# Optimization experiments

Measured on AMD Instinct MI355X. Metric: run time of the kernel, lower is better.

## Reference

```python
import jax, jax.numpy as jnp
import numpy as np

HEAD = 4
EPS = 1e-12


def _l2norm(x, axis):
    # torch F.normalize: x / max(||x||_2, eps)
    return x / jnp.maximum(jnp.linalg.norm(x, axis=axis, keepdims=True), EPS)


def setup_inputs() -> dict:
    key = jax.random.key(0)
    ks = jax.random.split(key, 12)
    n, t, c, h, w = 2, 7, 96, 96, 96
    inp = {
        "curr_feat": jax.random.normal(ks[0], (n, c, h, w), jnp.float32),
        "index_feat_set_s1": jax.random.normal(ks[1], (n, t, c, h, w), jnp.float32),
        "anchor_feat": jax.random.normal(ks[2], (n, c, h, w), jnp.float32),
        "sparse_feat_set_s1": jax.random.normal(ks[3], (n, t, c, h, w), jnp.float32),
        "sparse_feat_set_s2": jax.random.normal(ks[4], (n, t, c, h, w), jnp.float32),
        "sparse_feat_set_s3": jax.random.normal(ks[5], (n, t, c, h, w), jnp.float32),
        # absolute pixel coordinates (x,y interleaved per frame), mostly in-bounds
        # with a little overshoot to exercise zeros padding of grid_sample
        "location_feat": jax.random.uniform(ks[6], (n, t * 2, h, w), jnp.float32, minval=-2.0, maxval=float(w) + 1.0),
        "proj_w": 0.02 * jax.random.normal(ks[7], (c, c), jnp.float32),
        "proj_b": jnp.zeros((c,), jnp.float32),
        "fusion_w": 0.02 * jax.random.normal(ks[8], (c, 3 * c), jnp.float32),
        "fusion_b": jnp.zeros((c,), jnp.float32),
    }
    return inp


def reference(curr_feat, index_feat_set_s1, anchor_feat, sparse_feat_set_s1,
              sparse_feat_set_s2, sparse_feat_set_s3, location_feat,
              proj_w, proj_b, fusion_w, fusion_b):
    n, c, h, w = anchor_feat.shape
    t = sparse_feat_set_s1.shape[1]
    hd = c // HEAD
    hw = h * w

    # ---- flow-guided nearest grid_sample (align_corners=True, zeros pad) ----
    loc = location_feat.reshape(n, t, 2, h, w)  # (n,t,2,h,w): [x, y] pixel coords
    gx = 2.0 * loc[:, :, 0] / max(w - 1, 1) - 1.0
    gy = 2.0 * loc[:, :, 1] / max(h - 1, 1) - 1.0
    ix = jnp.round((gx + 1.0) * 0.5 * (w - 1))  # nearest (round-half-even, as torch)
    iy = jnp.round((gy + 1.0) * 0.5 * (h - 1))
    valid = (ix >= 0) & (ix <= w - 1) & (iy >= 0) & (iy <= h - 1)
    lin = (jnp.clip(iy, 0, h - 1).astype(jnp.int32) * w
           + jnp.clip(ix, 0, w - 1).astype(jnp.int32)).reshape(n, t, 1, hw)
    vmask = valid.reshape(n, t, 1, hw)

    def sample(f):  # f: (n,t,c,h,w) -> gathered (n,t,c,hw)
        g = jnp.take_along_axis(f.reshape(n, t, c, hw), lin, axis=3)
        return jnp.where(vmask, g, 0.0)

    samp1 = sample(sparse_feat_set_s1)
    samp2 = sample(sparse_feat_set_s2)
    samp3 = sample(sparse_feat_set_s3)
    sampi = sample(index_feat_set_s1)

    # ---- per-pixel multi-head max-correlation over t frames ----
    # queries: normalize over full channel dim c BEFORE splitting into heads
    q = _l2norm(curr_feat.reshape(n, c, hw).transpose(0, 2, 1), -1).reshape(n, hw, HEAD, hd)
    k = _l2norm(sampi.transpose(0, 3, 1, 2), -1).reshape(n, hw, t, HEAD, hd)
    scores = jnp.einsum('npthd,nphd->npht', k, q)  # scale == 1.0 in mode='max'
    corr_soft = jnp.max(scores, axis=3)     # (n,hw,head)
    corr_index = jnp.argmax(scores, axis=3)  # (n,hw,head), first-max like torch

    soft_img = jnp.broadcast_to(corr_soft[..., None], (n, hw, HEAD, hd)) \
                  .reshape(n, h, w, c).transpose(0, 3, 1, 2)  # (n,c,h,w)
    idx = jnp.broadcast_to(corr_index[..., None], (n, hw, HEAD, hd)) \
             .reshape(n, hw, c).transpose(0, 2, 1)[:, None]  # (n,1,c,hw)

    def pick(samp):  # select winning frame per (channel-group, pixel)
        return jnp.take_along_axis(samp, idx, axis=1)[:, 0].reshape(n, c, h, w)

    cat = jnp.concatenate([pick(samp1), pick(samp2), pick(samp3)], axis=1)  # (n,3c,h,w)
    out = jnp.einsum('ndhw,cd->nchw', cat, fusion_w) + fusion_b[None, :, None, None]
    out = out * soft_img
    out = jnp.einsum('nchw,dc->ndhw', out, proj_w) + proj_b[None, :, None, None]
    return out + anchor_feat
```

## Files before the change

### kernel.cpp

```cpp
#include <hip/hip_runtime.h>
#include <hip/hip_bf16.h>

#define N_    2
#define T_    7
#define C_    96
#define H_    96
#define W_    96
#define HW_   9216
#define HEAD_ 4
#define HD_   24
#define C3_   288
#define P_    16
#define QP_   100
#define CATP_ 292
#define NBLK_ (N_ * (HW_ / P_))
#define PLANES_ 14
#define CHUNK_  64
#define NCHUNK_ 144
#define TBLK_ (PLANES_ * NCHUNK_)

typedef unsigned int u32;

__device__ __forceinline__ float bits2f(u32 b) {
    union { u32 u; float f; } x; x.u = b; return x.f;
}

__device__ __forceinline__ unsigned short f2bf(float f) {
    union { __hip_bfloat16 h; unsigned short s; } u;
    u.h = __float2bfloat16(f);
    return u.s;
}

template<bool BF16>
__device__ __forceinline__ float ld1(const void* p, int i) {
    if constexpr (BF16) return bits2f(((u32)((const unsigned short*)p)[i]) << 16);
    else                return ((const float*)p)[i];
}

template<bool BF16>
__device__ __forceinline__ void ld4w(const void* p, int i, float w[4]) {
    if constexpr (BF16) {
        const uint2 u = ((const uint2*)p)[i >> 2];
        w[0] = bits2f(u.x << 16);
        w[1] = bits2f(u.x & 0xFFFF0000u);
        w[2] = bits2f(u.y << 16);
        w[3] = bits2f(u.y & 0xFFFF0000u);
    } else {
        const float4 v = *((const float4*)((const float*)p + i));
        w[0] = v.x; w[1] = v.y; w[2] = v.z; w[3] = v.w;
    }
}

template<bool BF16>
__device__ __forceinline__ void st1(void* p, int i, float v) {
    if constexpr (BF16) ((unsigned short*)p)[i] = f2bf(v);
    else                ((float*)p)[i] = v;
}

template<bool BF16>
__device__ __forceinline__ void st4w(void* p, int i, const float v[4]) {
    if constexpr (BF16) {
        uint2 w;
        w.x = (u32)f2bf(v[0]) | ((u32)f2bf(v[1]) << 16);
        w.y = (u32)f2bf(v[2]) | ((u32)f2bf(v[3]) << 16);
        ((uint2*)p)[i >> 2] = w;
    } else {
        *((float4*)((float*)p + i)) = make_float4(v[0], v[1], v[2], v[3]);
    }
}

__device__ __forceinline__ bool block_detect_bf16(const u32* __restrict__ w,
                                                  int tid, int* s_flag) {
    if (tid < 64) {
        u32 x = w[tid];
        u32 f = x & 0x7FFFu;
        int inwin = (f >= 0x3A00u) && (f <= 0x4200u);
        unsigned long long m = __ballot(inwin);
        if (tid == 0) *s_flag = (__popcll(m) >= 40) ? 1 : 0;
    }
    __syncthreads();
    return *s_flag != 0;
}

template<bool BF16>
__device__ __forceinline__ void transp_swz(const void* __restrict__ src,
                                           void* __restrict__ dst,
                                           int pl, int x0, int tid, char* raw) {
    if constexpr (BF16) {
        unsigned short* tile = (unsigned short*)raw;
        const unsigned short* s = (const unsigned short*)src;
        unsigned short* d = (unsigned short*)dst;
        for (int i = tid; i < C_ * (CHUNK_ / 4); i += 256) {
            int ch = i >> 4, xq = i & 15;
            const ushort4 v = *((const ushort4*)(s + (pl * C_ + ch) * HW_ + x0 + 4 * xq));
            int g = (ch >> 2) ^ (xq & 7);
            int chl = ch & 3;
            tile[(4 * xq + 0) * 96 + 4 * g + chl] = v.x;
            tile[(4 * xq + 1) * 96 + 4 * g + chl] = v.y;
            tile[(4 * xq + 2) * 96 + 4 * g + chl] = v.z;
            tile[(4 * xq + 3) * 96 + 4 * g + chl] = v.w;
        }
        __syncthreads();
        for (int i = tid; i < CHUNK_ * (C_ / 4); i += 256) {
            int p = i / 24, cq = i - p * 24;
            int g = cq ^ ((p >> 2) & 7);
            const ushort4 v = *((const ushort4*)&tile[p * 96 + 4 * g]);
            *((ushort4*)(d + (pl * HW_ + x0 + p) * C_ + 4 * cq)) = v;
        }
    } else {
        float* tile = (float*)raw;
        const float* s = (const float*)src;
        float* d = (float*)dst;
        for (int i = tid; i < C_ * (CHUNK_ / 4); i += 256) {
            int ch = i >> 4, xq = i & 15;
            const float4 v = *((const float4*)(s + (pl * C_ + ch) * HW_ + x0 + 4 * xq));
            int g = (ch >> 2) ^ (xq & 7);
            int chl = ch & 3;
            tile[(4 * xq + 0) * 96 + 4 * g + chl] = v.x;
            tile[(4 * xq + 1) * 96 + 4 * g + chl] = v.y;
            tile[(4 * xq + 2) * 96 + 4 * g + chl] = v.z;
            tile[(4 * xq + 3) * 96 + 4 * g + chl] = v.w;
        }
        __syncthreads();
        for (int i = tid; i < CHUNK_ * (C_ / 4); i += 256) {
            int p = i / 24, cq = i - p * 24;
            int g = cq ^ ((p >> 2) & 7);
            const float4 v = *((const float4*)&tile[p * 96 + 4 * g]);
            *((float4*)(d + (pl * HW_ + x0 + p) * C_ + 4 * cq)) = v;
        }
    }
}

__global__ __launch_bounds__(256) void transp_kernel(
    const void* __restrict__ a0, const void* __restrict__ a1,
    const void* __restrict__ a2, const void* __restrict__ a3,
    void* __restrict__ dstb, unsigned long long szb,
    const u32* __restrict__ detect_src)
{
    __shared__ __align__(16) char raw[24832];
    __shared__ int s_flag;
    const int arr = blockIdx.y;
    const void* src = (arr == 0) ? a0 : (arr == 1) ? a1 : (arr == 2) ? a2 : a3;
    void* dst = (char*)dstb + (unsigned long long)arr * szb;
    const int tid = threadIdx.x;
    const int pl = blockIdx.x / NCHUNK_;
    const int x0 = (blockIdx.x - pl * NCHUNK_) * CHUNK_;
    const bool bf = block_detect_bf16(detect_src, tid, &s_flag);
    if (bf) transp_swz<true >(src, dst, pl, x0, tid, raw);
    else    transp_swz<false>(src, dst, pl, x0, tid, raw);
}

template<bool BF16, bool TGB>
__device__ __forceinline__ void argmax_body(
    const void* __restrict__ curr, const void* __restrict__ loc,
    const void* __restrict__ kT,
    float* __restrict__ ws_best, int* __restrict__ ws_gbase,
    float* s_u, int (*s_lin)[P_], float (*s_red)[8],
    float (*s_best)[HEAD_], int (*s_bidx)[HEAD_], float* s_inv)
{
#define S_Q(pp, ch)  s_u[(pp) * QP_ + (ch)]
#define S_K(pp, ch)  s_u[P_ * QP_ + (pp) * QP_ + (ch)]
    const int tid = threadIdx.x;
    const int b  = blockIdx.x;
    const int nn = b / (HW_ / P_);
    const int p0 = (b - nn * (HW_ / P_)) * P_;

    if (tid < T_ * P_) {
        int t = tid / P_, pp = tid - t * P_;
        int p = p0 + pp;
        float x = ld1<BF16>(loc, (nn * 2 * T_ + 2 * t    ) * HW_ + p);
        float y = ld1<BF16>(loc, (nn * 2 * T_ + 2 * t + 1) * HW_ + p);
        float gx = 2.0f * x / 95.0f - 1.0f;
        float gy = 2.0f * y / 95.0f - 1.0f;
        float fx = (gx + 1.0f) * 0.5f * 95.0f;
        float fy = (gy + 1.0f) * 0.5f * 95.0f;
        float ix = rintf(fx), iy = rintf(fy);
        bool v = (ix >= 0.0f) && (ix <= 95.0f) && (iy >= 0.0f) && (iy <= 95.0f);
        s_lin[t][pp] = v ? ((int)iy * W_ + (int)ix) : -1;
    }
    if (tid >= 128 && tid < 128 + P_ * HEAD_) {
        int q = tid - 128;
        s_best[q >> 2][q & 3] = -3.0e38f; s_bidx[q >> 2][q & 3] = 0;
    }

    for (int i = tid; i < C_ * (P_ / 4); i += 256) {
        int ch = i >> 2, pq = i & 3;
        float w[4];
        ld4w<BF16>(curr, (nn * C_ + ch) * HW_ + p0 + 4 * pq, w);
        S_Q(4 * pq + 0, ch) = w[0]; S_Q(4 * pq + 1, ch) = w[1];
        S_Q(4 * pq + 2, ch) = w[2]; S_Q(4 * pq + 3, ch) = w[3];
    }
    __syncthreads();

    if (tid < P_ * 8) {
        int pp = tid >> 3, j = tid & 7;
        float s = 0.f;
        #pragma unroll
        for (int k = 0; k < 12; ++k) { float v = S_Q(pp, j * 12 + k); s += v * v; }
        s_red[pp][j] = s;
    }
    __syncthreads();
    if (tid < P_) {
        float s = 0.f;
        #pragma unroll
        for (int j = 0; j < 8; ++j) s += s_red[tid][j];
        s_inv[tid] = 1.0f / fmaxf(sqrtf(s), 1e-12f);
    }
    __syncthreads();
    for (int i = tid; i < C_ * P_; i += 256) {
        int pp = i & (P_ - 1), ch = i >> 4;
        S_Q(pp, ch) *= s_inv[pp];
    }

    for (int t = 0; t < T_; ++t) {
        __syncthreads();
        for (int i = tid; i < 24 * P_; i += 256) {
            int pp = i / 24, j = i - pp * 24;
            int lin = s_lin[t][pp];
            float w[4] = {0.f, 0.f, 0.f, 0.f};
            if (lin >= 0) ld4w<BF16>(kT, ((nn * T_ + t) * HW_ + lin) * C_ + 4 * j, w);
            *((float4*)&S_K(pp, 4 * j)) = make_float4(w[0], w[1], w[2], w[3]);
        }
        __syncthreads();
        if (tid < P_ * 8) {
            int pp = tid >> 3, j = tid & 7;
            float s = 0.f;
            #pragma unroll
            for (int k = 0; k < 12; ++k) { float v = S_K(pp, j * 12 + k); s += v * v; }
            s_red[pp][j] = s;
        }
        __syncthreads();
        if (tid < P_) {
            float s = 0.f;
            #pragma unroll
            for (int j = 0; j < 8; ++j) s += s_red[tid][j];
            s_inv[tid] = 1.0f / fmaxf(sqrtf(s), 1e-12f);
        }
        __syncthreads();
        if (tid < P_ * HEAD_) {
            int pp = tid >> 2, h = tid & 3;
            float s = 0.f;
            #pragma unroll
            for (int dq = 0; dq < 6; ++dq) {
                const float4 kv = *((const float4*)&S_K(pp, h * HD_ + 4 * dq));
                const float4 qv = *((const float4*)&S_Q(pp, h * HD_ + 4 * dq));
                s += kv.x * qv.x; s += kv.y * qv.y; s += kv.z * qv.z; s += kv.w * qv.w;
            }
            s *= s_inv[pp];
            if (s > s_best[pp][h]) { s_best[pp][h] = s; s_bidx[pp][h] = t; }
        }
    }
    if (tid < P_ * HEAD_) {
        int pp = tid >> 2, h = tid & 3;
        int bt = s_bidx[pp][h];
        int lin = s_lin[bt][pp];
        int g = (nn * HW_ + p0 + pp) * HEAD_ + h;
        ws_best[g] = s_best[pp][h];
        int gb;
        if (lin < 0)       gb = -1;
        else if (TGB)      gb = ((nn * T_ + bt) * HW_ + lin) * C_;
        else               gb = (nn * T_ + bt) * C_ * HW_ + lin;
        ws_gbase[g] = gb;
    }
#undef S_Q
#undef S_K
}

template<bool TGB>
__global__ __launch_bounds__(256, 8) void argmax_kernel(
    const void* __restrict__ curr, const void* __restrict__ loc,
    const void* __restrict__ kT,
    float* __restrict__ ws_best, int* __restrict__ ws_gbase)
{
    __shared__ __align__(16) float s_u[2 * P_ * QP_];
    __shared__ int   s_lin[T_][P_];
    __shared__ float s_red[P_][8];
    __shared__ float s_best[P_][HEAD_];
    __shared__ int   s_bidx[P_][HEAD_];
    __shared__ float s_inv[P_];
    __shared__ int   s_flag;
    const bool bf = block_detect_bf16((const u32*)curr, threadIdx.x, &s_flag);
    if (bf) argmax_body<true , TGB>(curr, loc, kT, ws_best, ws_gbase, s_u, s_lin, s_red, s_best, s_bidx, s_inv);
    else    argmax_body<false, TGB>(curr, loc, kT, ws_best, ws_gbase, s_u, s_lin, s_red, s_best, s_bidx, s_inv);
}

__global__ __launch_bounds__(256, 6) void fused_kernel(
    const void* __restrict__ curr, const void* __restrict__ loc,
    const void* __restrict__ kT,
    const void* __restrict__ s1, const void* __restrict__ s2,
    const void* __restrict__ s3,
    void* __restrict__ s123T, unsigned long long szb,
    float* __restrict__ ws_best, int* __restrict__ ws_gbase)
{
    __shared__ __align__(16) char raw[24832];
    __shared__ int s_flag;
    const int tid = threadIdx.x;
    const bool bf = block_detect_bf16((const u32*)curr, tid, &s_flag);
    const int bx = blockIdx.x;
    if (bx < NBLK_) {
        float* s_u            = (float*)raw;
        int   (*s_lin)[P_]    = (int(*)[P_])   (raw + 12800);
        float (*s_red)[8]     = (float(*)[8])  (raw + 13248);
        float (*s_best)[HEAD_]= (float(*)[HEAD_])(raw + 13760);
        int   (*s_bidx)[HEAD_]= (int(*)[HEAD_]) (raw + 14016);
        float* s_inv          = (float*)(raw + 14272);
        if (bf) argmax_body<true , true>(curr, loc, kT, ws_best, ws_gbase,
                                         s_u, s_lin, s_red, s_best, s_bidx, s_inv);
        else    argmax_body<false, true>(curr, loc, kT, ws_best, ws_gbase,
                                         s_u, s_lin, s_red, s_best, s_bidx, s_inv);
    } else {
        int t = bx - NBLK_;
        int arr = t / TBLK_;
        int bxx = t - arr * TBLK_;
        const void* src = (arr == 0) ? s1 : (arr == 1) ? s2 : s3;
        void* dst = (char*)s123T + (unsigned long long)arr * szb;
        int pl = bxx / NCHUNK_;
        int x0 = (bxx - pl * NCHUNK_) * CHUNK_;
        if (bf) transp_swz<true >(src, dst, pl, x0, tid, raw);
        else    transp_swz<false>(src, dst, pl, x0, tid, raw);
    }
}

template<bool BF16, bool TRANS>
__device__ __forceinline__ void catgemv_body(
    const void* __restrict__ anchor, const void* __restrict__ s1,
    const void* __restrict__ s2, const void* __restrict__ s3,
    const void* __restrict__ pw, const void* __restrict__ pb,
    const void* __restrict__ fw, const void* __restrict__ fb,
    void* __restrict__ outp,
    const float* __restrict__ ws_best, const int* __restrict__ ws_gbase,
    float* s_u, float (*s_mid)[QP_], float (*s_best)[HEAD_], int (*s_gbase)[HEAD_])
{
#define S_CAT(pp, d) s_u[(pp) * CATP_ + (d)]
    const int tid = threadIdx.x;
    const int b  = blockIdx.x;
    const int nn = b / (HW_ / P_);
    const int p0 = (b - nn * (HW_ / P_)) * P_;

    if (tid < P_ * HEAD_) {
        int pp = tid >> 2, h = tid & 3;
        int g = (nn * HW_ + p0 + pp) * HEAD_ + h;
        s_best[pp][h]  = ws_best[g];
        s_gbase[pp][h] = ws_gbase[g];
    }
    __syncthreads();

    if constexpr (TRANS) {
        for (int i = tid; i < P_ * 72; i += 256) {
            int px = i / 72, j = i - px * 72;
            int set = j / 24, jj = j - set * 24;
            int gb = s_gbase[px][jj / 6];
            float w[4] = {0.f, 0.f, 0.f, 0.f};
            if (gb >= 0) {
                const void* sp = (set == 0) ? s1 : (set == 1) ? s2 : s3;
                ld4w<BF16>(sp, gb + 4 * jj, w);
            }
            *((float4*)&S_CAT(px, set * C_ + 4 * jj)) = make_float4(w[0], w[1], w[2], w[3]);
        }
    } else {
        for (int i = tid; i < C3_ * P_; i += 256) {
            int pp = i / C3_, d = i - pp * C3_;
            int set = d / C_, ch = d - set * C_;
            int gb = s_gbase[pp][ch / HD_];
            float v = 0.f;
            if (gb >= 0) {
                const void* sp = (set == 0) ? s1 : (set == 1) ? s2 : s3;
                v = ld1<BF16>(sp, gb + ch * HW_);
            }
            S_CAT(pp, d) = v;
        }
    }
    __syncthreads();

    if (tid < 192) {
        const int cp = tid >> 2, pq = tid & 3;
        const int co0 = cp * 2, px0 = pq * 4;
        float acc[2][4];
        #pragma unroll
        for (int r = 0; r < 2; ++r)
            #pragma unroll
            for (int k = 0; k < 4; ++k) acc[r][k] = 0.f;
        for (int d = 0; d < C3_; d += 4) {
            float4 cv[4];
            #pragma unroll
            for (int k = 0; k < 4; ++k) cv[k] = *((const float4*)&S_CAT(px0 + k, d));
            #pragma unroll
            for (int r = 0; r < 2; ++r) {
                float w[4]; ld4w<BF16>(fw, (co0 + r) * C3_ + d, w);
                #pragma unroll
                for (int k = 0; k < 4; ++k)
                    acc[r][k] += w[0] * cv[k].x + w[1] * cv[k].y + w[2] * cv[k].z + w[3] * cv[k].w;
            }
        }
        const int hh = co0 / HD_;
        #pragma unroll
        for (int r = 0; r < 2; ++r) {
            float fbv = ld1<BF16>(fb, co0 + r);
            #pragma unroll
            for (int k = 0; k < 4; ++k)
                s_mid[px0 + k][co0 + r] = (acc[r][k] + fbv) * s_best[px0 + k][hh];
        }
    }
    __syncthreads();

    if (tid < 192) {
        const int dp = tid >> 2, pq = tid & 3;
        const int do0 = dp * 2, px0 = pq * 4;
        float acc[2][4];
        #pragma unroll
        for (int r = 0; r < 2; ++r)
            #pragma unroll
            for (int k = 0; k < 4; ++k) acc[r][k] = 0.f;
        for (int c = 0; c < C_; c += 4) {
            float4 mv[4];
            #pragma unroll
            for (int k = 0; k < 4; ++k) mv[k] = *((const float4*)&s_mid[px0 + k][c]);
            #pragma unroll
            for (int r = 0; r < 2; ++r) {
                float w[4]; ld4w<BF16>(pw, (do0 + r) * C_ + c, w);
                #pragma unroll
                for (int k = 0; k < 4; ++k)
                    acc[r][k] += w[0] * mv[k].x + w[1] * mv[k].y + w[2] * mv[k].z + w[3] * mv[k].w;
            }
        }
        #pragma unroll
        for (int r = 0; r < 2; ++r) {
            float pbv = ld1<BF16>(pb, do0 + r);
            float av[4];
            ld4w<BF16>(anchor, (nn * C_ + do0 + r) * HW_ + p0 + px0, av);
            float res[4];
            #pragma unroll
            for (int k = 0; k < 4; ++k) res[k] = acc[r][k] + pbv + av[k];
            st4w<BF16>(outp, (nn * C_ + do0 + r) * HW_ + p0 + px0, res);
        }
    }
#undef S_CAT
}

template<bool TRANS>
__global__ __launch_bounds__(256, 6) void catgemv_kernel(
    const void* __restrict__ curr, const void* __restrict__ anchor,
    const void* __restrict__ s1, const void* __restrict__ s2,
    const void* __restrict__ s3, const void* __restrict__ pw,
    const void* __restrict__ pb, const void* __restrict__ fw,
    const void* __restrict__ fb, void* __restrict__ outp,
    const float* __restrict__ ws_best, const int* __restrict__ ws_gbase)
{
    __shared__ __align__(16) float s_u[P_ * CATP_];
    __shared__ __align__(16) float s_mid[P_][QP_];
    __shared__ float s_best[P_][HEAD_];
    __shared__ int   s_gbase[P_][HEAD_];
    __shared__ int   s_flag;
    const bool bf = block_detect_bf16((const u32*)curr, threadIdx.x, &s_flag);
    if (bf) catgemv_body<true , TRANS>(anchor, s1, s2, s3, pw, pb, fw, fb, outp, ws_best, ws_gbase,
                                       s_u, s_mid, s_best, s_gbase);
    else    catgemv_body<false, TRANS>(anchor, s1, s2, s3, pw, pb, fw, fb, outp, ws_best, ws_gbase,
                                       s_u, s_mid, s_best, s_gbase);
}

template<bool BF16>
__device__ __forceinline__ void mono_body(
    const void* __restrict__ curr, const void* __restrict__ idxf,
    const void* __restrict__ anchor, const void* __restrict__ s1,
    const void* __restrict__ s2, const void* __restrict__ s3,
    const void* __restrict__ loc, const void* __restrict__ pw,
    const void* __restrict__ pb, const void* __restrict__ fw,
    const void* __restrict__ fb, void* __restrict__ outp,
    float* s_u, float (*s_mid)[QP_], int (*s_lin)[P_], float (*s_red)[8],
    float (*s_best)[HEAD_], int (*s_bidx)[HEAD_], float* s_inv)
{
#define S_Q(pp, ch)  s_u[(pp) * QP_ + (ch)]
#define S_K(pp, ch)  s_u[P_ * QP_ + (pp) * QP_ + (ch)]
#define S_CAT(pp, d) s_u[(pp) * CATP_ + (d)]
    const int tid = threadIdx.x;
    const int b  = blockIdx.x;
    const int nn = b / (HW_ / P_);
    const int p0 = (b - nn * (HW_ / P_)) * P_;

    if (tid < T_ * P_) {
        int t = tid / P_, pp = tid - t * P_;
        int p = p0 + pp;
        float x = ld1<BF16>(loc, (nn * 2 * T_ + 2 * t    ) * HW_ + p);
        float y = ld1<BF16>(loc, (nn * 2 * T_ + 2 * t + 1) * HW_ + p);
        float gx = 2.0f * x / 95.0f - 1.0f;
        float gy = 2.0f * y / 95.0f - 1.0f;
        float fx = (gx + 1.0f) * 0.5f * 95.0f;
        float fy = (gy + 1.0f) * 0.5f * 95.0f;
        float ix = rintf(fx), iy = rintf(fy);
        bool v = (ix >= 0.0f) && (ix <= 95.0f) && (iy >= 0.0f) && (iy <= 95.0f);
        s_lin[t][pp] = v ? ((int)iy * W_ + (int)ix) : -1;
    }
    if (tid >= 128 && tid < 128 + P_ * HEAD_) {
        int q = tid - 128;
        s_best[q >> 2][q & 3] = -3.0e38f; s_bidx[q >> 2][q & 3] = 0;
    }
    for (int i = tid; i < C_ * (P_ / 4); i += 256) {
        int ch = i >> 2, pq = i & 3;
        float w[4];
        ld4w<BF16>(curr, (nn * C_ + ch) * HW_ + p0 + 4 * pq, w);
        S_Q(4 * pq + 0, ch) = w[0]; S_Q(4 * pq + 1, ch) = w[1];
        S_Q(4 * pq + 2, ch) = w[2]; S_Q(4 * pq + 3, ch) = w[3];
    }
    __syncthreads();
    if (tid < P_ * 8) {
        int pp = tid >> 3, j = tid & 7;
        float s = 0.f;
        #pragma unroll
        for (int k = 0; k < 12; ++k) { float v = S_Q(pp, j * 12 + k); s += v * v; }
        s_red[pp][j] = s;
    }
    __syncthreads();
    if (tid < P_) {
        float s = 0.f;
        #pragma unroll
        for (int j = 0; j < 8; ++j) s += s_red[tid][j];
        s_inv[tid] = 1.0f / fmaxf(sqrtf(s), 1e-12f);
    }
    __syncthreads();
    for (int i = tid; i < C_ * P_; i += 256) {
        int pp = i & (P_ - 1), ch = i >> 4;
        S_Q(pp, ch) *= s_inv[pp];
    }
    for (int t = 0; t < T_; ++t) {
        __syncthreads();
        for (int i = tid; i < C_ * P_; i += 256) {
            int ch = i / P_, pp = i - ch * P_;
            int lin = s_lin[t][pp];
            S_K(pp, ch) = (lin >= 0) ? ld1<BF16>(idxf, ((nn * T_ + t) * C_ + ch) * HW_ + lin) : 0.0f;
        }
        __syncthreads();
        if (tid < P_ * 8) {
            int pp = tid >> 3, j = tid & 7;
            float s = 0.f;
            #pragma unroll
            for (int k = 0; k < 12; ++k) { float v = S_K(pp, j * 12 + k); s += v * v; }
            s_red[pp][j] = s;
        }
        __syncthreads();
        if (tid < P_) {
            float s = 0.f;
            #pragma unroll
            for (int j = 0; j < 8; ++j) s += s_red[tid][j];
            s_inv[tid] = 1.0f / fmaxf(sqrtf(s), 1e-12f);
        }
        __syncthreads();
        if (tid < P_ * HEAD_) {
            int pp = tid >> 2, h = tid & 3;
            float s = 0.f;
            #pragma unroll
            for (int dq = 0; dq < 6; ++dq) {
                const float4 kv = *((const float4*)&S_K(pp, h * HD_ + 4 * dq));
                const float4 qv = *((const float4*)&S_Q(pp, h * HD_ + 4 * dq));
                s += kv.x * qv.x; s += kv.y * qv.y; s += kv.z * qv.z; s += kv.w * qv.w;
            }
            s *= s_inv[pp];
            if (s > s_best[pp][h]) { s_best[pp][h] = s; s_bidx[pp][h] = t; }
        }
    }
    __syncthreads();
    for (int i = tid; i < C3_ * P_; i += 256) {
        int pp = i / C3_, d = i - pp * C3_;
        int set = d / C_, ch = d - set * C_;
        int h = ch / HD_;
        int bt = s_bidx[pp][h];
        int lin = s_lin[bt][pp];
        float v = 0.f;
        if (lin >= 0) {
            const void* sp = (set == 0) ? s1 : (set == 1) ? s2 : s3;
            v = ld1<BF16>(sp, ((nn * T_ + bt) * C_ + ch) * HW_ + lin);
        }
        S_CAT(pp, d) = v;
    }
    __syncthreads();
    if (tid < 96) {
        const int cq = tid >> 2, pq = tid & 3;
        const int co0 = cq * 4, px0 = pq * 4;
        float acc[4][4];
        #pragma unroll
        for (int r = 0; r < 4; ++r)
            #pragma unroll
            for (int k = 0; k < 4; ++k) acc[r][k] = 0.f;
        for (int d = 0; d < C3_; d += 4) {
            float4 cv[4];
            #pragma unroll
            for (int k = 0; k < 4; ++k) cv[k] = *((const float4*)&S_CAT(px0 + k, d));
            #pragma unroll
            for (int r = 0; r < 4; ++r) {
                float w[4]; ld4w<BF16>(fw, (co0 + r) * C3_ + d, w);
                #pragma unroll
                for (int k = 0; k < 4; ++k)
                    acc[r][k] += w[0] * cv[k].x + w[1] * cv[k].y + w[2] * cv[k].z + w[3] * cv[k].w;
            }
        }
        const int hh = co0 / HD_;
        #pragma unroll
        for (int r = 0; r < 4; ++r) {
            float fbv = ld1<BF16>(fb, co0 + r);
            #pragma unroll
            for (int k = 0; k < 4; ++k)
                s_mid[px0 + k][co0 + r] = (acc[r][k] + fbv) * s_best[px0 + k][hh];
        }
    }
    __syncthreads();
    if (tid < 96) {
        const int dq = tid >> 2, pq = tid & 3;
        const int do0 = dq * 4, px0 = pq * 4;
        float acc[4][4];
        #pragma unroll
        for (int r = 0; r < 4; ++r)
            #pragma unroll
            for (int k = 0; k < 4; ++k) acc[r][k] = 0.f;
        for (int c = 0; c < C_; c += 4) {
            float4 mv[4];
            #pragma unroll
            for (int k = 0; k < 4; ++k) mv[k] = *((const float4*)&s_mid[px0 + k][c]);
            #pragma unroll
            for (int r = 0; r < 4; ++r) {
                float w[4]; ld4w<BF16>(pw, (do0 + r) * C_ + c, w);
                #pragma unroll
                for (int k = 0; k < 4; ++k)
                    acc[r][k] += w[0] * mv[k].x + w[1] * mv[k].y + w[2] * mv[k].z + w[3] * mv[k].w;
            }
        }
        #pragma unroll
        for (int r = 0; r < 4; ++r) {
            float pbv = ld1<BF16>(pb, do0 + r);
            float av[4];
            ld4w<BF16>(anchor, (nn * C_ + do0 + r) * HW_ + p0 + px0, av);
            float res[4];
            #pragma unroll
            for (int k = 0; k < 4; ++k) res[k] = acc[r][k] + pbv + av[k];
            st4w<BF16>(outp, (nn * C_ + do0 + r) * HW_ + p0 + px0, res);
        }
    }
#undef S_Q
#undef S_K
#undef S_CAT
}

__global__ __launch_bounds__(256) void mono_kernel(
    const void* __restrict__ curr, const void* __restrict__ idxf,
    const void* __restrict__ anchor, const void* __restrict__ s1,
    const void* __restrict__ s2, const void* __restrict__ s3,
    const void* __restrict__ loc, const void* __restrict__ pw,
    const void* __restrict__ pb, const void* __restrict__ fw,
    const void* __restrict__ fb, void* __restrict__ outp)
{
    __shared__ __align__(16) float s_u[P_ * CATP_];
    __shared__ __align__(16) float s_mid[P_][QP_];
    __shared__ int   s_lin[T_][P_];
    __shared__ float s_red[P_][8];
    __shared__ float s_best[P_][HEAD_];
    __shared__ int   s_bidx[P_][HEAD_];
    __shared__ float s_inv[P_];
    __shared__ int   s_flag;
    const bool bf = block_detect_bf16((const u32*)curr, threadIdx.x, &s_flag);
    if (bf) mono_body<true >(curr, idxf, anchor, s1, s2, s3, loc, pw, pb, fw, fb, outp,
                             s_u, s_mid, s_lin, s_red, s_best, s_bidx, s_inv);
    else    mono_body<false>(curr, idxf, anchor, s1, s2, s3, loc, pw, pb, fw, fb, outp,
                             s_u, s_mid, s_lin, s_red, s_best, s_bidx, s_inv);
}

extern "C" void kernel_launch(void* const* d_in, const int* in_sizes, int n_in,
                              void* d_out, int out_size, void* d_ws, size_t ws_size,
                              hipStream_t stream) {
    (void)in_sizes; (void)n_in; (void)out_size;
    const unsigned long long SZB  = (unsigned long long)N_ * T_ * HW_ * C_ * 4ull;
    const unsigned long long AUXB = (unsigned long long)N_ * HW_ * HEAD_ * 4ull;
    char* wsb = (char*)d_ws;

    dim3 grid(NBLK_), block(256);
    if (ws_size >= 4 * SZB + 2 * AUXB) {
        void*  kT       = wsb;
        void*  s123T    = wsb + SZB;
        float* ws_best  = (float*)(wsb + 4 * SZB);
        int*   ws_gbase = (int*)  (wsb + 4 * SZB + AUXB);
        transp_kernel<<<dim3(TBLK_, 1), 256, 0, stream>>>(
            d_in[1], d_in[1], d_in[1], d_in[1], kT, SZB, (const u32*)d_in[0]);
        fused_kernel<<<dim3(NBLK_ + 3 * TBLK_), 256, 0, stream>>>(
            d_in[0], d_in[6], kT, d_in[3], d_in[4], d_in[5], s123T, SZB, ws_best, ws_gbase);
        catgemv_kernel<true><<<grid, block, 0, stream>>>(
            d_in[0], d_in[2],
            (char*)s123T, (char*)s123T + SZB, (char*)s123T + 2 * SZB,
            d_in[7], d_in[8], d_in[9], d_in[10], d_out, ws_best, ws_gbase);
    } else if (ws_size >= SZB + 2 * AUXB) {
        void*  kT       = wsb;
        float* ws_best  = (float*)(wsb + SZB);
        int*   ws_gbase = (int*)  (wsb + SZB + AUXB);
        transp_kernel<<<dim3(TBLK_, 1), 256, 0, stream>>>(
            d_in[1], d_in[1], d_in[1], d_in[1], kT, SZB, (const u32*)d_in[0]);
        argmax_kernel<false><<<grid, block, 0, stream>>>(d_in[0], d_in[6], kT, ws_best, ws_gbase);
        catgemv_kernel<false><<<grid, block, 0, stream>>>(d_in[0], d_in[2], d_in[3], d_in[4], d_in[5],
                                                          d_in[7], d_in[8], d_in[9], d_in[10],
                                                          d_out, ws_best, ws_gbase);
    } else {
        mono_kernel<<<grid, block, 0, stream>>>(d_in[0], d_in[1], d_in[2], d_in[3], d_in[4],
                                                d_in[5], d_in[6], d_in[7], d_in[8], d_in[9],
                                                d_in[10], d_out);
    }
}
```

Baseline: 302.5 us.

## Prefetch next-frame keys in registers and shrink transpose chunks for occupancy

```diff
diff --git a/kernel.cpp b/kernel.cpp
--- a/kernel.cpp
+++ b/kernel.cpp
@@ -15,8 +15,8 @@
 #define CATP_ 292
 #define NBLK_ (N_ * (HW_ / P_))
 #define PLANES_ 14
-#define CHUNK_  64
-#define NCHUNK_ 144
+#define CHUNK_  48
+#define NCHUNK_ 192
 #define TBLK_ (PLANES_ * NCHUNK_)
 
 typedef unsigned int u32;
@@ -91,7 +91,7 @@
         const unsigned short* s = (const unsigned short*)src;
         unsigned short* d = (unsigned short*)dst;
         for (int i = tid; i < C_ * (CHUNK_ / 4); i += 256) {
-            int ch = i >> 4, xq = i & 15;
+            int ch = i / 12, xq = i - ch * 12;
             const ushort4 v = *((const ushort4*)(s + (pl * C_ + ch) * HW_ + x0 + 4 * xq));
             int g = (ch >> 2) ^ (xq & 7);
             int chl = ch & 3;
@@ -112,7 +112,7 @@
         const float* s = (const float*)src;
         float* d = (float*)dst;
         for (int i = tid; i < C_ * (CHUNK_ / 4); i += 256) {
-            int ch = i >> 4, xq = i & 15;
+            int ch = i / 12, xq = i - ch * 12;
             const float4 v = *((const float4*)(s + (pl * C_ + ch) * HW_ + x0 + 4 * xq));
             int g = (ch >> 2) ^ (xq & 7);
             int chl = ch & 3;
@@ -137,7 +137,7 @@
     void* __restrict__ dstb, unsigned long long szb,
     const u32* __restrict__ detect_src)
 {
-    __shared__ __align__(16) char raw[24832];
+    __shared__ __align__(16) char raw[CHUNK_ * 96 * 4];
     __shared__ int s_flag;
     const int arr = blockIdx.y;
     const void* src = (arr == 0) ? a0 : (arr == 1) ? a1 : (arr == 2) ? a2 : a3;
@@ -212,14 +212,39 @@
         S_Q(pp, ch) *= s_inv[pp];
     }
 
+    const int pp0 = tid / 24,        j0 = tid - pp0 * 24;
+    const int pp1 = (tid + 256) / 24, j1 = (tid + 256) - pp1 * 24;
+    const bool has1 = (tid < 128);
+
+    float4 ka0, ka1;
+    {
+        int lin = s_lin[0][pp0];
+        float w[4] = {0.f, 0.f, 0.f, 0.f};
+        if (lin >= 0) ld4w<BF16>(kT, ((nn * T_) * HW_ + lin) * C_ + 4 * j0, w);
+        ka0 = make_float4(w[0], w[1], w[2], w[3]);
+        if (has1) {
+            int lin2 = s_lin[0][pp1];
+            float w2[4] = {0.f, 0.f, 0.f, 0.f};
+            if (lin2 >= 0) ld4w<BF16>(kT, ((nn * T_) * HW_ + lin2) * C_ + 4 * j1, w2);
+            ka1 = make_float4(w2[0], w2[1], w2[2], w2[3]);
+        }
+    }
+
     for (int t = 0; t < T_; ++t) {
         __syncthreads();
-        for (int i = tid; i < 24 * P_; i += 256) {
-            int pp = i / 24, j = i - pp * 24;
-            int lin = s_lin[t][pp];
+        *((float4*)&S_K(pp0, 4 * j0)) = ka0;
+        if (has1) *((float4*)&S_K(pp1, 4 * j1)) = ka1;
+        if (t + 1 < T_) {
+            int lin = s_lin[t + 1][pp0];
             float w[4] = {0.f, 0.f, 0.f, 0.f};
-            if (lin >= 0) ld4w<BF16>(kT, ((nn * T_ + t) * HW_ + lin) * C_ + 4 * j, w);
-            *((float4*)&S_K(pp, 4 * j)) = make_float4(w[0], w[1], w[2], w[3]);
+            if (lin >= 0) ld4w<BF16>(kT, ((nn * T_ + t + 1) * HW_ + lin) * C_ + 4 * j0, w);
+            ka0 = make_float4(w[0], w[1], w[2], w[3]);
+            if (has1) {
+                int lin2 = s_lin[t + 1][pp1];
+                float w2[4] = {0.f, 0.f, 0.f, 0.f};
+                if (lin2 >= 0) ld4w<BF16>(kT, ((nn * T_ + t + 1) * HW_ + lin2) * C_ + 4 * j1, w2);
+                ka1 = make_float4(w2[0], w2[1], w2[2], w2[3]);
+            }
         }
         __syncthreads();
         if (tid < P_ * 8) {
@@ -284,7 +309,7 @@
     else    argmax_body<false, TGB>(curr, loc, kT, ws_best, ws_gbase, s_u, s_lin, s_red, s_best, s_bidx, s_inv);
 }
 
-__global__ __launch_bounds__(256, 6) void fused_kernel(
+__global__ __launch_bounds__(256, 8) void fused_kernel(
     const void* __restrict__ curr, const void* __restrict__ loc,
     const void* __restrict__ kT,
     const void* __restrict__ s1, const void* __restrict__ s2,
@@ -292,7 +317,7 @@
     void* __restrict__ s123T, unsigned long long szb,
     float* __restrict__ ws_best, int* __restrict__ ws_gbase)
 {
-    __shared__ __align__(16) char raw[24832];
+    __shared__ __align__(16) char raw[CHUNK_ * 96 * 4];
     __shared__ int s_flag;
     const int tid = threadIdx.x;
     const bool bf = block_detect_bf16((const u32*)curr, tid, &s_flag);
```

New measurement: 307.2 us. No clear change (+1.5%).
